# Performance work log

Hardware: AMD Instinct MI355X
Metric: run time of the kernel (lower is better)

The kernel has to match this reference:

```python
import jax, jax.numpy as jnp
import numpy as np

R = 8
EPS = 1e-08
EPSS = 1e-12


def _diff_x(x, r):
    left = x[:, :, r:2 * r + 1]
    middle = x[:, :, 2 * r + 1:] - x[:, :, :-2 * r - 1]
    right = x[:, :, -1:] - x[:, :, -2 * r - 1:-r - 1]
    return jnp.concatenate([left, middle, right], axis=2)


def _diff_y(x, r):
    left = x[:, :, :, r:2 * r + 1]
    middle = x[:, :, :, 2 * r + 1:] - x[:, :, :, :-2 * r - 1]
    right = x[:, :, :, -1:] - x[:, :, :, -2 * r - 1:-r - 1]
    return jnp.concatenate([left, middle, right], axis=3)


def box_filter(x, r):
    # cumsum-based (2r+1)x(2r+1) box sum with clamped borders (matches torch BoxFilter)
    return _diff_y(jnp.cumsum(_diff_x(jnp.cumsum(x, axis=2), r), axis=3), r)


def bilinear_resize(x, H, W):
    # F.interpolate(mode='bilinear', align_corners=True) for NCHW
    n, c, h, w = x.shape
    ys = jnp.linspace(0.0, h - 1.0, H)
    xs = jnp.linspace(0.0, w - 1.0, W)
    y0 = jnp.floor(ys).astype(jnp.int32)
    x0 = jnp.floor(xs).astype(jnp.int32)
    y1 = jnp.minimum(y0 + 1, h - 1)
    x1 = jnp.minimum(x0 + 1, w - 1)
    wy = (ys - y0).astype(x.dtype)[None, None, :, None]
    wx = (xs - x0).astype(x.dtype)[None, None, None, :]
    rows = jnp.take(x, y0, axis=2) * (1.0 - wy) + jnp.take(x, y1, axis=2) * wy
    return jnp.take(rows, x0, axis=3) * (1.0 - wx) + jnp.take(rows, x1, axis=3) * wx


def setup_inputs() -> dict:
    key = jax.random.key(0)
    k1, k2, k3, k4 = jax.random.split(key, 4)
    return {
        "lr_x": jax.random.normal(k1, (4, 3, 256, 256), dtype=jnp.float32),
        "lr_y": jax.random.normal(k2, (4, 3, 256, 256), dtype=jnp.float32),
        "hr_x": jax.random.normal(k3, (4, 3, 1024, 1024), dtype=jnp.float32),
        "l_a": jax.random.uniform(k4, (4, 3, 256, 256), dtype=jnp.float32),
    }


def reference(lr_x, lr_y, hr_x, l_a):
    n, c, h, w = lr_x.shape
    _, _, hh, wh = hr_x.shape
    dt = lr_x.dtype

    N = box_filter(jnp.ones((1, 1, h, w), dtype=dt), R)  # local window counts

    l_a = jnp.abs(l_a) + EPSS
    l_t = l_a / jnp.sum(l_a)

    mean_a = box_filter(l_a) if False else box_filter(l_a, R) / N
    mean_a2xy = box_filter(l_a * l_a * lr_x * lr_y, R) / N
    mean_tax = box_filter(l_t * l_a * lr_x, R) / N
    mean_ay = box_filter(l_a * lr_y, R) / N
    mean_a2x2 = box_filter(l_a * l_a * lr_x * lr_x, R) / N
    mean_ax = box_filter(l_a * lr_x, R) / N

    temp = jnp.abs(mean_a2x2 - N * mean_tax * mean_ax)
    A = (mean_a2xy - N * mean_tax * mean_ay) / (temp + EPS)
    b = (mean_ay - A * mean_ax) / mean_a

    A = box_filter(A, R) / N
    b = box_filter(b, R) / N

    mean_A = bilinear_resize(A, hh, wh)
    mean_b = bilinear_resize(b, hh, wh)
    return (mean_A * hr_x + mean_b).astype(jnp.float32)
```

## Files before the change

kernel.cpp:

```cpp
#include <hip/hip_runtime.h>

#define RAD 8
#define HH 256
#define WW 256
#define NC 12
#define PS (HH*WW)

__device__ __forceinline__ int swz(int b) { return (b & 7) * 96 + (b >> 3); }

__global__ __launch_bounds__(256) void k_hbox6(const float* __restrict__ la,
                                               const float* __restrict__ lx,
                                               const float* __restrict__ ly,
                                               float* __restrict__ Hbuf,
                                               float* __restrict__ partials) {
    int c  = swz(blockIdx.x);
    int p  = c >> 6;
    int rc = c & 63;
    int base = p * PS + rc * 4 * WW;
    int tid = threadIdx.x, lane = tid & 63, wid = tid >> 6;
    __shared__ float wtot[6][4];
    __shared__ float Pref[6][WW];
    __shared__ float ls[4];
    float asum = 0.0f;
    int  j1    = min(tid + RAD, WW - 1);
    bool hasj0 = (tid - RAD) > 0;
    int  j0m1  = tid - RAD - 1;
    for (int rr = 0; rr < 4; rr++) {
        int o = base + rr * WW + tid;
        float a  = fabsf(la[o]) + 1e-12f;
        float xv = lx[o];
        float yv = ly[o];
        asum += a;
        float ax = a * xv, ay = a * yv;
        float v0 = a, v1 = ax, v2 = ay, v3 = a * ax, v4 = ax * ax, v5 = ax * ay;
        #pragma unroll
        for (int off = 1; off < 64; off <<= 1) {
            float t0 = __shfl_up(v0, off, 64), t1 = __shfl_up(v1, off, 64),
                  t2 = __shfl_up(v2, off, 64), t3 = __shfl_up(v3, off, 64),
                  t4 = __shfl_up(v4, off, 64), t5 = __shfl_up(v5, off, 64);
            if (lane >= off) { v0 += t0; v1 += t1; v2 += t2; v3 += t3; v4 += t4; v5 += t5; }
        }
        if (lane == 63) {
            wtot[0][wid] = v0; wtot[1][wid] = v1; wtot[2][wid] = v2;
            wtot[3][wid] = v3; wtot[4][wid] = v4; wtot[5][wid] = v5;
        }
        __syncthreads();
        float a0 = 0, a1 = 0, a2 = 0, a3 = 0, a4 = 0, a5 = 0;
        for (int w = 0; w < wid; w++) {
            a0 += wtot[0][w]; a1 += wtot[1][w]; a2 += wtot[2][w];
            a3 += wtot[3][w]; a4 += wtot[4][w]; a5 += wtot[5][w];
        }
        Pref[0][tid] = v0 + a0; Pref[1][tid] = v1 + a1; Pref[2][tid] = v2 + a2;
        Pref[3][tid] = v3 + a3; Pref[4][tid] = v4 + a4; Pref[5][tid] = v5 + a5;
        __syncthreads();
        #pragma unroll
        for (int k = 0; k < 6; k++) {
            float s = Pref[k][j1] - (hasj0 ? Pref[k][j0m1] : 0.0f);
            Hbuf[k * NC * PS + o] = s;
        }
    }
    for (int off = 32; off > 0; off >>= 1) asum += __shfl_down(asum, off, 64);
    if (lane == 0) ls[wid] = asum;
    __syncthreads();
    if (tid == 0) partials[blockIdx.x] = ls[0] + ls[1] + ls[2] + ls[3];
}

__global__ __launch_bounds__(256) void k_vab(const float* __restrict__ Hbuf,
                                             const float* __restrict__ partials,
                                             float* __restrict__ HA,
                                             float* __restrict__ HB) {
    int c  = swz(blockIdx.x);
    int p  = c >> 6;
    int i0 = (c & 63) * 4;
    int tid = threadIdx.x, lane = tid & 63, wid = tid >> 6;
    __shared__ float wtot[2][4];
    __shared__ float Pref[2][WW];
    __shared__ float ls[4];
    __shared__ float sS;

    float psum = partials[tid] + partials[tid + 256] + partials[tid + 512];
    for (int off = 32; off > 0; off >>= 1) psum += __shfl_down(psum, off, 64);
    if (lane == 0) ls[wid] = psum;
    __syncthreads();
    if (tid == 0) sS = ls[0] + ls[1] + ls[2] + ls[3];
    __syncthreads();
    float invS = 1.0f / sS;

    const float* Hp = Hbuf + p * PS + tid;
    float s0 = 0, s1 = 0, s2 = 0, s3 = 0, s4 = 0, s5 = 0;
    int lo = max(i0 - RAD, 0), hi = min(i0 + RAD, HH - 1);
    for (int i = lo; i <= hi; i++) {
        int o = i * WW;
        s0 += Hp[0 * NC * PS + o]; s1 += Hp[1 * NC * PS + o]; s2 += Hp[2 * NC * PS + o];
        s3 += Hp[3 * NC * PS + o]; s4 += Hp[4 * NC * PS + o]; s5 += Hp[5 * NC * PS + o];
    }
    float cx = (float)(min(tid + RAD, WW - 1) - max(tid - RAD, 0) + 1);
    int  j1c   = min(tid + RAD, WW - 1);
    bool hasj0 = (tid - RAD) > 0;
    int  j0m1  = tid - RAD - 1;
    for (int i = i0; i < i0 + 4; i++) {
        if (i > i0) {
            int add = i + RAD, sub = i - RAD - 1;
            if (add <= HH - 1) {
                int o = add * WW;
                s0 += Hp[0 * NC * PS + o]; s1 += Hp[1 * NC * PS + o]; s2 += Hp[2 * NC * PS + o];
                s3 += Hp[3 * NC * PS + o]; s4 += Hp[4 * NC * PS + o]; s5 += Hp[5 * NC * PS + o];
            }
            if (sub >= 0) {
                int o = sub * WW;
                s0 -= Hp[0 * NC * PS + o]; s1 -= Hp[1 * NC * PS + o]; s2 -= Hp[2 * NC * PS + o];
                s3 -= Hp[3 * NC * PS + o]; s4 -= Hp[4 * NC * PS + o]; s5 -= Hp[5 * NC * PS + o];
            }
        }
        float cy = (float)(min(i + RAD, HH - 1) - max(i - RAD, 0) + 1);
        float Nv = cx * cy;
        float invN = 1.0f / Nv;
        float mean_a    = s0 * invN;
        float mean_ax   = s1 * invN;
        float mean_ay   = s2 * invN;
        float mean_tax  = s3 * invN * invS;
        float mean_a2x2 = s4 * invN;
        float mean_a2xy = s5 * invN;
        float temp = fabsf(mean_a2x2 - Nv * mean_tax * mean_ax);
        float Av = (mean_a2xy - Nv * mean_tax * mean_ay) / (temp + 1e-8f);
        float bv = (mean_ay - Av * mean_ax) / mean_a;

        float v0 = Av, v1 = bv;
        #pragma unroll
        for (int off = 1; off < 64; off <<= 1) {
            float t0 = __shfl_up(v0, off, 64), t1 = __shfl_up(v1, off, 64);
            if (lane >= off) { v0 += t0; v1 += t1; }
        }
        if (lane == 63) { wtot[0][wid] = v0; wtot[1][wid] = v1; }
        __syncthreads();
        float a0 = 0, a1 = 0;
        for (int w = 0; w < wid; w++) { a0 += wtot[0][w]; a1 += wtot[1][w]; }
        Pref[0][tid] = v0 + a0; Pref[1][tid] = v1 + a1;
        __syncthreads();
        int o = p * PS + i * WW + tid;
        HA[o] = Pref[0][j1c] - (hasj0 ? Pref[0][j0m1] : 0.0f);
        HB[o] = Pref[1][j1c] - (hasj0 ? Pref[1][j0m1] : 0.0f);
    }
}

__global__ __launch_bounds__(256) void k_vbox2(const float* __restrict__ HA,
                                               const float* __restrict__ HB,
                                               float* __restrict__ mA,
                                               float* __restrict__ mB) {
    int c  = swz(blockIdx.x);
    int p  = c >> 6;
    int i0 = (c & 63) * 4;
    int col = threadIdx.x;
    const float* a = HA + p * PS + col;
    const float* b = HB + p * PS + col;
    float sa = 0, sb = 0;
    int lo = max(i0 - RAD, 0), hi = min(i0 + RAD, HH - 1);
    for (int i = lo; i <= hi; i++) { sa += a[i * WW]; sb += b[i * WW]; }
    float cx = (float)(min(col + RAD, WW - 1) - max(col - RAD, 0) + 1);
    for (int i = i0; i < i0 + 4; i++) {
        if (i > i0) {
            if (i + RAD <= HH - 1) { sa += a[(i + RAD) * WW]; sb += b[(i + RAD) * WW]; }
            if (i - RAD - 1 >= 0)  { sa -= a[(i - RAD - 1) * WW]; sb -= b[(i - RAD - 1) * WW]; }
        }
        float cy = (float)(min(i + RAD, HH - 1) - max(i - RAD, 0) + 1);
        float inv = 1.0f / (cx * cy);
        mA[p * PS + i * WW + col] = sa * inv;
        mB[p * PS + i * WW + col] = sb * inv;
    }
}

__global__ __launch_bounds__(256) void k_resize(const float* __restrict__ mA,
                                                const float* __restrict__ mB,
                                                const float* __restrict__ hrx,
                                                float* __restrict__ out) {
    int idx = blockIdx.x * 256 + threadIdx.x;
    int p   = idx >> 18;
    int rem = idx & ((1 << 18) - 1);
    int I   = rem >> 8;
    int J4  = (rem & 255) << 2;
    const float scale = 255.0f / 1023.0f;
    float ysf = (float)I * scale;
    int   y0  = (int)ysf;
    float wy  = ysf - (float)y0;
    int   y1  = min(y0 + 1, HH - 1);
    const float* a0p = mA + p * PS + y0 * WW;
    const float* a1p = mA + p * PS + y1 * WW;
    const float* b0p = mB + p * PS + y0 * WW;
    const float* b1p = mB + p * PS + y1 * WW;
    int xb = (int)((float)J4 * scale);
    int i1 = min(xb + 1, WW - 1);
    int i2 = min(xb + 2, WW - 1);
    float A0a = a0p[xb], A0b = a0p[i1], A0c = a0p[i2];
    float A1a = a1p[xb], A1b = a1p[i1], A1c = a1p[i2];
    float B0a = b0p[xb], B0b = b0p[i1], B0c = b0p[i2];
    float B1a = b1p[xb], B1b = b1p[i1], B1c = b1p[i2];
    float4 h = ((const float4*)hrx)[idx];
    float hv[4] = {h.x, h.y, h.z, h.w};
    float ov[4];
    float omwy = 1.0f - wy;
    #pragma unroll
    for (int k = 0; k < 4; k++) {
        float xsk = (float)(J4 + k) * scale;
        int   x0  = (int)xsk;
        float wx  = xsk - (float)x0;
        bool hisel = (x0 > xb);
        float Alo0 = hisel ? A0b : A0a, Ahi0 = hisel ? A0c : A0b;
        float Alo1 = hisel ? A1b : A1a, Ahi1 = hisel ? A1c : A1b;
        float Blo0 = hisel ? B0b : B0a, Bhi0 = hisel ? B0c : B0b;
        float Blo1 = hisel ? B1b : B1a, Bhi1 = hisel ? B1c : B1b;
        float omwx = 1.0f - wx;
        float Ar0 = Alo0 * omwx + Ahi0 * wx;
        float Ar1 = Alo1 * omwx + Ahi1 * wx;
        float Br0 = Blo0 * omwx + Bhi0 * wx;
        float Br1 = Blo1 * omwx + Bhi1 * wx;
        float Avv = Ar0 * omwy + Ar1 * wy;
        float Bvv = Br0 * omwy + Br1 * wy;
        ov[k] = Avv * hv[k] + Bvv;
    }
    float4 o;
    o.x = ov[0]; o.y = ov[1]; o.z = ov[2]; o.w = ov[3];
    ((float4*)out)[idx] = o;
}

extern "C" void kernel_launch(void* const* d_in, const int* in_sizes, int n_in,
                              void* d_out, int out_size, void* d_ws, size_t ws_size,
                              hipStream_t stream) {
    const float* lr_x = (const float*)d_in[0];
    const float* lr_y = (const float*)d_in[1];
    const float* hr_x = (const float*)d_in[2];
    const float* l_a  = (const float*)d_in[3];
    float* out = (float*)d_out;

    float* ws       = (float*)d_ws;
    float* partials = ws;
    float* Hbuf     = ws + 1024;
    float* HA       = Hbuf + 6 * NC * PS;
    float* HB       = HA + NC * PS;
    float* mA       = HB + NC * PS;
    float* mB       = mA + NC * PS;

    k_hbox6 <<<NC * 64, 256, 0, stream>>>(l_a, lr_x, lr_y, Hbuf, partials);
    k_vab   <<<NC * 64, 256, 0, stream>>>(Hbuf, partials, HA, HB);
    k_vbox2 <<<NC * 64, 256, 0, stream>>>(HA, HB, mA, mB);
    k_resize<<<(NC * 1024 * 1024 / 4) / 256, 256, 0, stream>>>(mA, mB, hr_x, out);
}
```

Baseline: 151.1 us.

## Fuse box filters and A/b computation into one banded per-wave kernel

Replaces the three kernels for the horizontal box, A/b computation and second box with a separate sum reduction followed by a single fused kernel. Each wavefront handles a 32-column strip with a 16-column halo over an 8-row band. It keeps a running vertical sum in registers and does the horizontal 17-wide sums with wave shuffles, and a per-wave LDS ring buffer holds the second vertical box. This removes the 6-channel Hbuf and the HA/HB intermediate round-trips through global memory. In exchange it recomputes halo rows and columns, with only half the lanes producing output and 24 rows of input read per 8 output rows.

```diff
diff --git a/kernel.cpp b/kernel.cpp
--- a/kernel.cpp
+++ b/kernel.cpp
@@ -8,165 +8,136 @@
 
 __device__ __forceinline__ int swz(int b) { return (b & 7) * 96 + (b >> 3); }
 
-__global__ __launch_bounds__(256) void k_hbox6(const float* __restrict__ la,
-                                               const float* __restrict__ lx,
-                                               const float* __restrict__ ly,
-                                               float* __restrict__ Hbuf,
-                                               float* __restrict__ partials) {
-    int c  = swz(blockIdx.x);
-    int p  = c >> 6;
-    int rc = c & 63;
-    int base = p * PS + rc * 4 * WW;
-    int tid = threadIdx.x, lane = tid & 63, wid = tid >> 6;
-    __shared__ float wtot[6][4];
-    __shared__ float Pref[6][WW];
+__device__ __forceinline__ float run17(float x) {
+    float s = x + __shfl_up(x, 1, 64);
+    s += __shfl_up(s, 2, 64);
+    s += __shfl_up(s, 4, 64);
+    s += __shfl_up(s, 8, 64);
+    s += __shfl_up(x, 16, 64);
+    return s;
+}
+
+__global__ __launch_bounds__(256) void k_reduce(const float* __restrict__ la,
+                                                float* __restrict__ partials) {
+    int tid = threadIdx.x;
     __shared__ float ls[4];
-    float asum = 0.0f;
-    int  j1    = min(tid + RAD, WW - 1);
-    bool hasj0 = (tid - RAD) > 0;
-    int  j0m1  = tid - RAD - 1;
-    for (int rr = 0; rr < 4; rr++) {
-        int o = base + rr * WW + tid;
-        float a  = fabsf(la[o]) + 1e-12f;
-        float xv = lx[o];
-        float yv = ly[o];
-        asum += a;
-        float ax = a * xv, ay = a * yv;
-        float v0 = a, v1 = ax, v2 = ay, v3 = a * ax, v4 = ax * ax, v5 = ax * ay;
-        #pragma unroll
-        for (int off = 1; off < 64; off <<= 1) {
-            float t0 = __shfl_up(v0, off, 64), t1 = __shfl_up(v1, off, 64),
-                  t2 = __shfl_up(v2, off, 64), t3 = __shfl_up(v3, off, 64),
-                  t4 = __shfl_up(v4, off, 64), t5 = __shfl_up(v5, off, 64);
-            if (lane >= off) { v0 += t0; v1 += t1; v2 += t2; v3 += t3; v4 += t4; v5 += t5; }
-        }
-        if (lane == 63) {
-            wtot[0][wid] = v0; wtot[1][wid] = v1; wtot[2][wid] = v2;
-            wtot[3][wid] = v3; wtot[4][wid] = v4; wtot[5][wid] = v5;
-        }
-        __syncthreads();
-        float a0 = 0, a1 = 0, a2 = 0, a3 = 0, a4 = 0, a5 = 0;
-        for (int w = 0; w < wid; w++) {
-            a0 += wtot[0][w]; a1 += wtot[1][w]; a2 += wtot[2][w];
-            a3 += wtot[3][w]; a4 += wtot[4][w]; a5 += wtot[5][w];
-        }
-        Pref[0][tid] = v0 + a0; Pref[1][tid] = v1 + a1; Pref[2][tid] = v2 + a2;
-        Pref[3][tid] = v3 + a3; Pref[4][tid] = v4 + a4; Pref[5][tid] = v5 + a5;
-        __syncthreads();
-        #pragma unroll
-        for (int k = 0; k < 6; k++) {
-            float s = Pref[k][j1] - (hasj0 ? Pref[k][j0m1] : 0.0f);
-            Hbuf[k * NC * PS + o] = s;
-        }
+    const float4* p4 = (const float4*)la;
+    int base = blockIdx.x * 2048 + tid;
+    float s = 0.f;
+    #pragma unroll
+    for (int i = 0; i < 8; i++) {
+        float4 v = p4[base + i * 256];
+        s += (fabsf(v.x) + 1e-12f) + (fabsf(v.y) + 1e-12f) +
+             (fabsf(v.z) + 1e-12f) + (fabsf(v.w) + 1e-12f);
     }
-    for (int off = 32; off > 0; off >>= 1) asum += __shfl_down(asum, off, 64);
-    if (lane == 0) ls[wid] = asum;
+    for (int off = 32; off > 0; off >>= 1) s += __shfl_down(s, off, 64);
+    int lane = tid & 63, wid = tid >> 6;
+    if (lane == 0) ls[wid] = s;
     __syncthreads();
     if (tid == 0) partials[blockIdx.x] = ls[0] + ls[1] + ls[2] + ls[3];
 }
 
-__global__ __launch_bounds__(256) void k_vab(const float* __restrict__ Hbuf,
-                                             const float* __restrict__ partials,
-                                             float* __restrict__ HA,
-                                             float* __restrict__ HB) {
-    int c  = swz(blockIdx.x);
-    int p  = c >> 6;
-    int i0 = (c & 63) * 4;
-    int tid = threadIdx.x, lane = tid & 63, wid = tid >> 6;
-    __shared__ float wtot[2][4];
-    __shared__ float Pref[2][WW];
-    __shared__ float ls[4];
-    __shared__ float sS;
-
-    float psum = partials[tid] + partials[tid + 256] + partials[tid + 512];
-    for (int off = 32; off > 0; off >>= 1) psum += __shfl_down(psum, off, 64);
-    if (lane == 0) ls[wid] = psum;
-    __syncthreads();
-    if (tid == 0) sS = ls[0] + ls[1] + ls[2] + ls[3];
-    __syncthreads();
-    float invS = 1.0f / sS;
-
-    const float* Hp = Hbuf + p * PS + tid;
+__global__ __launch_bounds__(256) void k_band(const float* __restrict__ la,
+                                              const float* __restrict__ lx,
+                                              const float* __restrict__ ly,
+                                              const float* __restrict__ partials,
+                                              float* __restrict__ mA,
+                                              float* __restrict__ mB) {
+    __shared__ float2 ring[4][17][64];
+    int tid = threadIdx.x, lane = tid & 63, wv = tid >> 6;
+    int gw  = swz(blockIdx.x) * 4 + wv;
+    int p   = gw >> 8;
+    int rem = gw & 255;
+    int cp  = rem & 7, rb = rem >> 3;
+    int i0  = rb << 3;
+    int col = (cp << 5) - 16 + lane;
+    bool vc = (col >= 0) && (col < WW);
+    int colc = min(max(col, 0), WW - 1);
+    const float* pa = la + p * PS + colc;
+    const float* px = lx + p * PS + colc;
+    const float* py = ly + p * PS + colc;
+
+    float psum = partials[lane] + ((lane < 32) ? partials[lane + 64] : 0.0f);
+    #pragma unroll
+    for (int off = 32; off > 0; off >>= 1) psum += __shfl_xor(psum, off, 64);
+    float invS = 1.0f / psum;
+
+    int  cA  = col - 8;
+    bool vcA = (cA >= 0) && (cA < WW);
+    float cxA = (float)(min(cA + RAD, WW - 1) - max(cA - RAD, 0) + 1);
+    int   cM  = col - 16;
+    float cxM = (float)(min(cM + RAD, WW - 1) - max(cM - RAD, 0) + 1);
+
     float s0 = 0, s1 = 0, s2 = 0, s3 = 0, s4 = 0, s5 = 0;
-    int lo = max(i0 - RAD, 0), hi = min(i0 + RAD, HH - 1);
-    for (int i = lo; i <= hi; i++) {
-        int o = i * WW;
-        s0 += Hp[0 * NC * PS + o]; s1 += Hp[1 * NC * PS + o]; s2 += Hp[2 * NC * PS + o];
-        s3 += Hp[3 * NC * PS + o]; s4 += Hp[4 * NC * PS + o]; s5 += Hp[5 * NC * PS + o];
-    }
-    float cx = (float)(min(tid + RAD, WW - 1) - max(tid - RAD, 0) + 1);
-    int  j1c   = min(tid + RAD, WW - 1);
-    bool hasj0 = (tid - RAD) > 0;
-    int  j0m1  = tid - RAD - 1;
-    for (int i = i0; i < i0 + 4; i++) {
-        if (i > i0) {
-            int add = i + RAD, sub = i - RAD - 1;
-            if (add <= HH - 1) {
-                int o = add * WW;
-                s0 += Hp[0 * NC * PS + o]; s1 += Hp[1 * NC * PS + o]; s2 += Hp[2 * NC * PS + o];
-                s3 += Hp[3 * NC * PS + o]; s4 += Hp[4 * NC * PS + o]; s5 += Hp[5 * NC * PS + o];
+    auto accum = [&](int r, float sg) {
+        float va = 0.f, vx = 0.f, vy = 0.f;
+        if (vc) { int o = r * WW; va = pa[o]; vx = px[o]; vy = py[o]; }
+        float a  = vc ? (fabsf(va) + 1e-12f) : 0.f;
+        float ax = a * vx, ay = a * vy;
+        s0 = fmaf(sg, a, s0); s1 = fmaf(sg, ax, s1); s2 = fmaf(sg, ay, s2);
+        s3 = fmaf(sg, a * ax, s3); s4 = fmaf(sg, ax * ax, s4); s5 = fmaf(sg, ax * ay, s5);
+    };
+
+    #pragma unroll 1
+    for (int r = i0 - 16; r <= i0; ++r)
+        if (r >= 0) accum(r, 1.0f);
+
+    float tA = 0.f, tB = 0.f;
+    int slot = 0;
+
+    auto midrow = [&](int m, bool doOld, bool doInit, bool doOut) {
+        if (m > i0 - 8) {
+            int ra = m + 8; if (ra < HH) accum(ra, 1.0f);
+            int rs = m - 9; if (rs >= 0) accum(rs, -1.0f);
+        }
+        float h0 = run17(s0), h1 = run17(s1), h2 = run17(s2),
+              h3 = run17(s3), h4 = run17(s4), h5 = run17(s5);
+        float Av = 0.f, bv = 0.f;
+        if (m >= 0 && m < HH) {
+            float cy = (float)(min(m + RAD, HH - 1) - max(m - RAD, 0) + 1);
+            float Nv = cxA * cy, invN = 1.0f / Nv;
+            float m_a = h0 * invN, m_ax = h1 * invN, m_ay = h2 * invN;
+            float m_tax = h3 * invN * invS;
+            float m_a2x2 = h4 * invN, m_a2xy = h5 * invN;
+            float tempv = fabsf(m_a2x2 - Nv * m_tax * m_ax);
+            float Avt = (m_a2xy - Nv * m_tax * m_ay) / (tempv + 1e-8f);
+            float bvt = (m_ay - Avt * m_ax) / m_a;
+            if (vcA) { Av = Avt; bv = bvt; }
+        }
+        if (doOld) {
+            float2 old = ring[wv][slot][lane];
+            tA += Av - old.x; tB += bv - old.y;
+        }
+        float2 cur; cur.x = Av; cur.y = bv;
+        ring[wv][slot][lane] = cur;
+        if (doInit) {
+            tA = Av; tB = bv;
+            #pragma unroll
+            for (int k = 0; k < 16; ++k) {
+                int sl = slot + 1 + k; if (sl >= 17) sl -= 17;
+                float2 v = ring[wv][sl][lane];
+                tA += v.x; tB += v.y;
             }
-            if (sub >= 0) {
-                int o = sub * WW;
-                s0 -= Hp[0 * NC * PS + o]; s1 -= Hp[1 * NC * PS + o]; s2 -= Hp[2 * NC * PS + o];
-                s3 -= Hp[3 * NC * PS + o]; s4 -= Hp[4 * NC * PS + o]; s5 -= Hp[5 * NC * PS + o];
+        }
+        if (doOut) {
+            int o = m - 8;
+            float HtA = run17(tA), HtB = run17(tB);
+            float cy2 = (float)(min(o + RAD, HH - 1) - max(o - RAD, 0) + 1);
+            float inv2 = 1.0f / (cxM * cy2);
+            if (lane >= 32) {
+                int off = p * PS + o * WW + cM;
+                mA[off] = HtA * inv2;
+                mB[off] = HtB * inv2;
             }
         }
-        float cy = (float)(min(i + RAD, HH - 1) - max(i - RAD, 0) + 1);
-        float Nv = cx * cy;
-        float invN = 1.0f / Nv;
-        float mean_a    = s0 * invN;
-        float mean_ax   = s1 * invN;
-        float mean_ay   = s2 * invN;
-        float mean_tax  = s3 * invN * invS;
-        float mean_a2x2 = s4 * invN;
-        float mean_a2xy = s5 * invN;
-        float temp = fabsf(mean_a2x2 - Nv * mean_tax * mean_ax);
-        float Av = (mean_a2xy - Nv * mean_tax * mean_ay) / (temp + 1e-8f);
-        float bv = (mean_ay - Av * mean_ax) / mean_a;
-
-        float v0 = Av, v1 = bv;
-        #pragma unroll
-        for (int off = 1; off < 64; off <<= 1) {
-            float t0 = __shfl_up(v0, off, 64), t1 = __shfl_up(v1, off, 64);
-            if (lane >= off) { v0 += t0; v1 += t1; }
-        }
-        if (lane == 63) { wtot[0][wid] = v0; wtot[1][wid] = v1; }
-        __syncthreads();
-        float a0 = 0, a1 = 0;
-        for (int w = 0; w < wid; w++) { a0 += wtot[0][w]; a1 += wtot[1][w]; }
-        Pref[0][tid] = v0 + a0; Pref[1][tid] = v1 + a1;
-        __syncthreads();
-        int o = p * PS + i * WW + tid;
-        HA[o] = Pref[0][j1c] - (hasj0 ? Pref[0][j0m1] : 0.0f);
-        HB[o] = Pref[1][j1c] - (hasj0 ? Pref[1][j0m1] : 0.0f);
-    }
-}
-
-__global__ __launch_bounds__(256) void k_vbox2(const float* __restrict__ HA,
-                                               const float* __restrict__ HB,
-                                               float* __restrict__ mA,
-                                               float* __restrict__ mB) {
-    int c  = swz(blockIdx.x);
-    int p  = c >> 6;
-    int i0 = (c & 63) * 4;
-    int col = threadIdx.x;
-    const float* a = HA + p * PS + col;
-    const float* b = HB + p * PS + col;
-    float sa = 0, sb = 0;
-    int lo = max(i0 - RAD, 0), hi = min(i0 + RAD, HH - 1);
-    for (int i = lo; i <= hi; i++) { sa += a[i * WW]; sb += b[i * WW]; }
-    float cx = (float)(min(col + RAD, WW - 1) - max(col - RAD, 0) + 1);
-    for (int i = i0; i < i0 + 4; i++) {
-        if (i > i0) {
-            if (i + RAD <= HH - 1) { sa += a[(i + RAD) * WW]; sb += b[(i + RAD) * WW]; }
-            if (i - RAD - 1 >= 0)  { sa -= a[(i - RAD - 1) * WW]; sb -= b[(i - RAD - 1) * WW]; }
-        }
-        float cy = (float)(min(i + RAD, HH - 1) - max(i - RAD, 0) + 1);
-        float inv = 1.0f / (cx * cy);
-        mA[p * PS + i * WW + col] = sa * inv;
-        mB[p * PS + i * WW + col] = sb * inv;
-    }
+        slot = (slot == 16) ? 0 : slot + 1;
+    };
+
+    #pragma unroll 1
+    for (int m = i0 - 8; m <= i0 + 7; ++m) midrow(m, false, false, false);
+    midrow(i0 + 8, false, true, true);
+    #pragma unroll 1
+    for (int m = i0 + 9; m <= i0 + 15; ++m) midrow(m, true, false, true);
 }
 
 __global__ __launch_bounds__(256) void k_resize(const float* __restrict__ mA,
@@ -233,14 +204,10 @@
 
     float* ws       = (float*)d_ws;
     float* partials = ws;
-    float* Hbuf     = ws + 1024;
-    float* HA       = Hbuf + 6 * NC * PS;
-    float* HB       = HA + NC * PS;
-    float* mA       = HB + NC * PS;
+    float* mA       = ws + 256;
     float* mB       = mA + NC * PS;
 
-    k_hbox6 <<<NC * 64, 256, 0, stream>>>(l_a, lr_x, lr_y, Hbuf, partials);
-    k_vab   <<<NC * 64, 256, 0, stream>>>(Hbuf, partials, HA, HB);
-    k_vbox2 <<<NC * 64, 256, 0, stream>>>(HA, HB, mA, mB);
+    k_reduce<<<96, 256, 0, stream>>>(l_a, partials);
+    k_band  <<<768, 256, 0, stream>>>(l_a, lr_x, lr_y, partials, mA, mB);
     k_resize<<<(NC * 1024 * 1024 / 4) / 256, 256, 0, stream>>>(mA, mB, hr_x, out);
 }
```

New measurement: 162.5 us. 7.5% more time.
